# Kernel optimization log

Hardware: AMD Instinct MI355X
Metric: run time of the kernel (lower is better)

Reference implementation:

```python
import jax, jax.numpy as jnp
import numpy as np

N_USER, N_REST, D, E, Q = 200000, 50000, 64, 2000000, 500000


def setup_inputs() -> dict:
    key = jax.random.key(0)
    ks = jax.random.split(key, 16)
    s = 0.05
    return {
        "x_user": jax.random.normal(ks[0], (N_USER, D), jnp.float32),
        "x_rest": jax.random.normal(ks[1], (N_REST, D), jnp.float32),
        "Wl": jax.random.normal(ks[2], (3, 2, D, D), jnp.float32) * s,
        "Wr": jax.random.normal(ks[3], (3, 2, D, D), jnp.float32) * s,
        "bl": jnp.zeros((3, 2, D), jnp.float32),
        "dW1": jax.random.normal(ks[4], (D, 2 * D), jnp.float32) * s,
        "db1": jnp.zeros((D,), jnp.float32),
        "dW2": jax.random.normal(ks[5], (D, D), jnp.float32) * s,
        "db2": jnp.zeros((D,), jnp.float32),
        "dW3": jax.random.normal(ks[6], (1, D), jnp.float32) * s,
        "db3": jnp.zeros((1,), jnp.float32),
        "ur_src": jax.random.randint(ks[7], (E,), 0, N_USER, jnp.int32),
        "ur_dst": jax.random.randint(ks[8], (E,), 0, N_REST, jnp.int32),
        "ru_src": jax.random.randint(ks[9], (E,), 0, N_REST, jnp.int32),
        "ru_dst": jax.random.randint(ks[10], (E,), 0, N_USER, jnp.int32),
        "el_row": jax.random.randint(ks[11], (Q,), 0, N_USER, jnp.int32),
        "el_col": jax.random.randint(ks[12], (Q,), 0, N_REST, jnp.int32),
    }


def _sage(h_src, h_dst, src, dst, W_l, b_l, W_r):
    # PyG SAGEConv: lin_l(mean_{j in N(i)} x_j) + lin_r(x_i); bias on lin_l only.
    n_dst = h_dst.shape[0]
    agg = jax.ops.segment_sum(h_src[src], dst, num_segments=n_dst)  # [n_dst, D]
    cnt = jax.ops.segment_sum(jnp.ones_like(dst, dtype=h_src.dtype), dst, num_segments=n_dst)
    mean = agg / jnp.maximum(cnt, 1)[:, None]
    return mean @ W_l.T + b_l + h_dst @ W_r.T


def reference(x_user, x_rest, Wl, Wr, bl, dW1, db1, dW2, db2, dW3, db3,
              ur_src, ur_dst, ru_src, ru_dst, el_row, el_col):
    hu, hr = x_user, x_rest
    for l in range(3):
        # edge type 0: user -> restaurant ('rates'); edge type 1: reverse
        zr = _sage(hu, hr, ur_src, ur_dst, Wl[l, 0], bl[l, 0], Wr[l, 0])
        zu = _sage(hr, hu, ru_src, ru_dst, Wl[l, 1], bl[l, 1], Wr[l, 1])
        if l < 2:
            zr, zu = jax.nn.relu(zr), jax.nn.relu(zu)
        hu, hr = zu, zr
    # EdgeDecoder
    z = jnp.concatenate([hu[el_row], hr[el_col]], axis=-1)  # [Q, 2D]
    z = jax.nn.relu(z @ dW1.T + db1)
    z = jax.nn.relu(z @ dW2.T + db2)
    z = z @ dW3.T + db3
    return z.reshape(-1)
```

## Files before the change

kernel.cpp:

```cpp
#include <hip/hip_runtime.h>

#define NU 200000
#define NR 50000
#define DD 64
#define NE 2000000
#define NQ 500000
#define NBR 196
#define NBU 782

#define NBS 98
#define BKT_CAP 24576
#define LW_U 11
#define LW_R 9
#define PB_E 4096
#define NPBB 489

__global__ __launch_bounds__(256)
void binpass_kernel(const int* __restrict__ ru_src, const int* __restrict__ ru_dst,
                    const int* __restrict__ ur_src, const int* __restrict__ ur_dst,
                    int* __restrict__ bcur, int2* __restrict__ pairs) {
    __shared__ int2 stg[PB_E];
    __shared__ unsigned char gstg[PB_E];
    __shared__ int hist[256];
    __shared__ int sca[256], scb[256];
    __shared__ int gpos[128];
    int side = (blockIdx.x >= NPBB) ? 1 : 0;
    int blk = side ? (blockIdx.x - NPBB) : blockIdx.x;
    const int* src = side ? ur_src : ru_src;
    const int* dst = side ? ur_dst : ru_dst;
    int lw = side ? LW_R : LW_U;
    int* bc = bcur + side * NBS;
    int2* region = pairs + (size_t)side * NBS * BKT_CAP;
    int tid = threadIdx.x;
    hist[tid] = 0;
    __syncthreads();
    int base = blk * PB_E;
    int myg[16]; int myrank[16]; int2 myp[16];
#pragma unroll
    for (int i = 0; i < 16; i++) {
        int e = base + i * 256 + tid;
        if (e < NE) {
            int d = dst[e];
            int g = d >> lw;
            myg[i] = g;
            myp[i] = make_int2(src[e], d);
            myrank[i] = atomicAdd(&hist[g], 1);
        } else myg[i] = -1;
    }
    __syncthreads();
    int h = hist[tid];
    sca[tid] = h;
    __syncthreads();
    int* cur = sca; int* alt = scb;
    for (int off = 1; off < 256; off <<= 1) {
        int x = cur[tid];
        if (tid >= off) x += cur[tid - off];
        alt[tid] = x;
        __syncthreads();
        int* tmp = cur; cur = alt; alt = tmp;
    }
    alt[tid] = cur[tid] - h;
    if (tid < NBS && h > 0) gpos[tid] = atomicAdd(&bc[tid], h);
    __syncthreads();
    int* basep = alt;
#pragma unroll
    for (int i = 0; i < 16; i++) {
        if (myg[i] >= 0) {
            int p = basep[myg[i]] + myrank[i];
            stg[p] = myp[i];
            gstg[p] = (unsigned char)myg[i];
        }
    }
    __syncthreads();
    int tot = cur[255];
    for (int i = tid; i < tot; i += 256) {
        int g = gstg[i];
        int o = g * BKT_CAP + gpos[g] + (i - basep[g]);
        region[o] = stg[i];
    }
}

__global__ void bbase_kernel(const int* __restrict__ bcur, int* __restrict__ bbase,
                             int* __restrict__ rs_u, int* __restrict__ rs_r) {
    __shared__ int a[128], b[128];
    int sidx = blockIdx.x;
    const int* bc = bcur + sidx * NBS;
    int* bb = bbase + sidx * NBS;
    int tid = threadIdx.x;
    a[tid] = (tid < NBS) ? bc[tid] : 0;
    __syncthreads();
    int* cur = a; int* alt = b;
    for (int off = 1; off < 128; off <<= 1) {
        int t = cur[tid];
        if (tid >= off) t += cur[tid - off];
        alt[tid] = t;
        __syncthreads();
        int* tmp = cur; cur = alt; alt = tmp;
    }
    if (tid < NBS) bb[tid] = (tid == 0) ? 0 : cur[tid - 1];
    if (tid == 0) { if (sidx == 0) rs_u[NU] = NE; else rs_r[NR] = NE; }
}

__global__ __launch_bounds__(256)
void fillpass_kernel(const int2* __restrict__ pairs, const int* __restrict__ bcur,
                     const int* __restrict__ bbase,
                     int* __restrict__ rs_u, int* __restrict__ rs_r,
                     int* __restrict__ csr_u, int* __restrict__ csr_r) {
    __shared__ int win[BKT_CAP];
    __shared__ int lcnt[2048];
    __shared__ int lofs[2048];
    __shared__ int tsc[256], tsc2[256];
    int side = (blockIdx.x >= NBS) ? 1 : 0;
    int bkt = side ? (blockIdx.x - NBS) : blockIdx.x;
    const int2* reg = pairs + ((size_t)side * NBS + bkt) * BKT_CAP;
    int* rs = side ? rs_r : rs_u;
    int* csr = side ? csr_r : csr_u;
    int W = side ? 512 : 2048;
    int lw = side ? LW_R : LW_U;
    int n = side ? NR : NU;
    int d0 = bkt << lw;
    int tot = bcur[side * NBS + bkt];
    int base = bbase[side * NBS + bkt];
    int tid = threadIdx.x;
    for (int i = tid; i < W; i += 256) lcnt[i] = 0;
    __syncthreads();
    for (int i = tid; i < tot; i += 256) {
        int2 p = reg[i];
        atomicAdd(&lcnt[p.y - d0], 1);
    }
    __syncthreads();
    int per = W >> 8;
    int b0 = tid * per;
    int run = 0;
    for (int i = 0; i < per; i++) { int v = lcnt[b0 + i]; lofs[b0 + i] = run; run += v; }
    tsc[tid] = run;
    __syncthreads();
    int* cur = tsc; int* alt = tsc2;
    for (int off = 1; off < 256; off <<= 1) {
        int x = cur[tid];
        if (tid >= off) x += cur[tid - off];
        alt[tid] = x;
        __syncthreads();
        int* tmp = cur; cur = alt; alt = tmp;
    }
    int texcl = cur[tid] - run;
    for (int i = 0; i < per; i++) lofs[b0 + i] += texcl;
    __syncthreads();
    int wn = min(W, n - d0);
    for (int i = tid; i < wn; i += 256) rs[d0 + i] = base + lofs[i];
    __syncthreads();
    for (int i = tid; i < tot; i += 256) {
        int2 p = reg[i];
        int slot = atomicAdd(&lofs[p.y - d0], 1);
        win[slot] = p.x;
    }
    __syncthreads();
    for (int i = tid; i < tot; i += 256) csr[base + i] = win[i];
}

__global__ __launch_bounds__(256)
void gather2_kernel(const float* __restrict__ hu, const int* __restrict__ csr_r,
                    const int* __restrict__ rs_r, float* __restrict__ mean_r,
                    const float* __restrict__ hr, const int* __restrict__ csr_u,
                    const int* __restrict__ rs_u, float* __restrict__ mean_u) {
    int lane = threadIdx.x & 63;
    int wave = blockIdx.x * 4 + (threadIdx.x >> 6);
    const float* h; const int* csr; const int* rs; float* mean; int r;
    if (wave < NR) { h = hu; csr = csr_r; rs = rs_r; mean = mean_r; r = wave; }
    else if (wave < NR + NU) { h = hr; csr = csr_u; rs = rs_u; mean = mean_u; r = wave - NR; }
    else return;
    int s = rs[r], e = rs[r + 1];
    int g = lane >> 4;
    int fo = (lane & 15) << 2;
    float4 a0 = {0.f, 0.f, 0.f, 0.f};
    float4 a1 = {0.f, 0.f, 0.f, 0.f};
    for (int j = s; j < e; j += 64) {
        int rem = e - j;
        int nch = rem < 64 ? rem : 64;
        int li = lane < nch ? lane : nch - 1;
        int idx = csr[j + li];
        for (int kk = 0; kk < nch; kk += 8) {
            int j0 = kk + g;
            int j1 = kk + 4 + g;
            int i0 = __shfl(idx, j0);
            int i1 = __shfl(idx, j1);
            float4 x0 = *(const float4*)(h + (size_t)i0 * DD + fo);
            float4 x1 = *(const float4*)(h + (size_t)i1 * DD + fo);
            if (j0 < nch) { a0.x += x0.x; a0.y += x0.y; a0.z += x0.z; a0.w += x0.w; }
            if (j1 < nch) { a1.x += x1.x; a1.y += x1.y; a1.z += x1.z; a1.w += x1.w; }
        }
    }
    float4 acc;
    acc.x = a0.x + a1.x; acc.y = a0.y + a1.y;
    acc.z = a0.z + a1.z; acc.w = a0.w + a1.w;
    acc.x += __shfl_xor(acc.x, 16); acc.y += __shfl_xor(acc.y, 16);
    acc.z += __shfl_xor(acc.z, 16); acc.w += __shfl_xor(acc.w, 16);
    acc.x += __shfl_xor(acc.x, 32); acc.y += __shfl_xor(acc.y, 32);
    acc.z += __shfl_xor(acc.z, 32); acc.w += __shfl_xor(acc.w, 32);
    if (g == 0) {
        float inv = 1.0f / fmaxf((float)(e - s), 1.0f);
        acc.x *= inv; acc.y *= inv; acc.z *= inv; acc.w *= inv;
        *(float4*)(mean + (size_t)r * DD + fo) = acc;
    }
}

#define DOT4(A, B) ((A).x*(B).x + (A).y*(B).y + (A).z*(B).z + (A).w*(B).w)

#define SDECL(j) float sA##j = bsh[cb + (j)], sB##j = sA##j, sC##j = sA##j, sD##j = sA##j;

#define SCOL(j) { \
    const float4* wlp_ = (const float4*)(Wls + ((cb + (j)) << 6) + kc); \
    const float4* wrp_ = (const float4*)(Wrs + ((cb + (j)) << 6) + kc); \
    float4 l0_ = wlp_[0], l1_ = wlp_[1], q0_ = wrp_[0], q1_ = wrp_[1]; \
    sA##j += DOT4(mA0,l0_)+DOT4(mA1,l1_)+DOT4(xA0,q0_)+DOT4(xA1,q1_); \
    sB##j += DOT4(mB0,l0_)+DOT4(mB1,l1_)+DOT4(xB0,q0_)+DOT4(xB1,q1_); \
    sC##j += DOT4(mC0,l0_)+DOT4(mC1,l1_)+DOT4(xC0,q0_)+DOT4(xC1,q1_); \
    sD##j += DOT4(mD0,l0_)+DOT4(mD1,l1_)+DOT4(xD0,q0_)+DOT4(xD1,q1_); }

#define SRELU(j) { sA##j = fmaxf(sA##j,0.f); sB##j = fmaxf(sB##j,0.f); \
                   sC##j = fmaxf(sC##j,0.f); sD##j = fmaxf(sD##j,0.f); }

#define STORE_ROW(SR, rr) if ((rr) < n) { \
    float* o_ = out + (size_t)(rr) * DD + cb; \
    *(float4*)(o_)      = {SR##0,  SR##1,  SR##2,  SR##3}; \
    *(float4*)(o_ + 4)  = {SR##4,  SR##5,  SR##6,  SR##7}; \
    *(float4*)(o_ + 8)  = {SR##8,  SR##9,  SR##10, SR##11}; \
    *(float4*)(o_ + 12) = {SR##12, SR##13, SR##14, SR##15}; }

__device__ __forceinline__
void sage_tile(const float* __restrict__ mean, const float* __restrict__ h,
               const float* Wls, const float* Wrs, const float* bsh,
               float* __restrict__ out, int n, int do_relu, int r0, int cb) {
    int rA = min(r0, n - 1), rB = min(r0 + 64, n - 1);
    int rC = min(r0 + 128, n - 1), rD = min(r0 + 192, n - 1);
    const float *mA = mean + (size_t)rA * DD, *xA = h + (size_t)rA * DD;
    const float *mB = mean + (size_t)rB * DD, *xB = h + (size_t)rB * DD;
    const float *mC = mean + (size_t)rC * DD, *xC = h + (size_t)rC * DD;
    const float *mD = mean + (size_t)rD * DD, *xD = h + (size_t)rD * DD;
    SDECL(0)  SDECL(1)  SDECL(2)  SDECL(3)  SDECL(4)  SDECL(5)  SDECL(6)  SDECL(7)
    SDECL(8)  SDECL(9)  SDECL(10) SDECL(11) SDECL(12) SDECL(13) SDECL(14) SDECL(15)
#pragma unroll 1
    for (int kc = 0; kc < DD; kc += 8) {
        float4 mA0 = *(const float4*)(mA + kc), mA1 = *(const float4*)(mA + kc + 4);
        float4 xA0 = *(const float4*)(xA + kc), xA1 = *(const float4*)(xA + kc + 4);
        float4 mB0 = *(const float4*)(mB + kc), mB1 = *(const float4*)(mB + kc + 4);
        float4 xB0 = *(const float4*)(xB + kc), xB1 = *(const float4*)(xB + kc + 4);
        float4 mC0 = *(const float4*)(mC + kc), mC1 = *(const float4*)(mC + kc + 4);
        float4 xC0 = *(const float4*)(xC + kc), xC1 = *(const float4*)(xC + kc + 4);
        float4 mD0 = *(const float4*)(mD + kc), mD1 = *(const float4*)(mD + kc + 4);
        float4 xD0 = *(const float4*)(xD + kc), xD1 = *(const float4*)(xD + kc + 4);
        SCOL(0)  SCOL(1)  SCOL(2)  SCOL(3)  SCOL(4)  SCOL(5)  SCOL(6)  SCOL(7)
        SCOL(8)  SCOL(9)  SCOL(10) SCOL(11) SCOL(12) SCOL(13) SCOL(14) SCOL(15)
    }
    if (do_relu) {
        SRELU(0)  SRELU(1)  SRELU(2)  SRELU(3)  SRELU(4)  SRELU(5)  SRELU(6)  SRELU(7)
        SRELU(8)  SRELU(9)  SRELU(10) SRELU(11) SRELU(12) SRELU(13) SRELU(14) SRELU(15)
    }
    STORE_ROW(sA, r0)
    STORE_ROW(sB, r0 + 64)
    STORE_ROW(sC, r0 + 128)
    STORE_ROW(sD, r0 + 192)
}

__global__ __launch_bounds__(256, 2)
void sage_fused_kernel(const float* __restrict__ mean_r, const float* __restrict__ hr,
                       const float* __restrict__ mean_u, const float* __restrict__ hu,
                       const float* __restrict__ Wl2, const float* __restrict__ Wr2,
                       const float* __restrict__ bl2,
                       float* __restrict__ out_r, float* __restrict__ out_u, int do_relu) {
    __shared__ float Wls[DD * DD];
    __shared__ float Wrs[DD * DD];
    __shared__ float bsh[DD];
    int side = (blockIdx.x < NBR) ? 0 : 1;
    const float* Wl = Wl2 + side * DD * DD;
    const float* Wr = Wr2 + side * DD * DD;
    const float* bl = bl2 + side * DD;
    for (int i = threadIdx.x; i < DD * DD; i += 256) {
        Wls[i] = Wl[i];
        Wrs[i] = Wr[i];
    }
    if (threadIdx.x < DD) bsh[threadIdx.x] = bl[threadIdx.x];
    __syncthreads();
    int lane = threadIdx.x & 63;
    int cb = (threadIdx.x >> 6) * 16;
    if (side == 0) {
        int r0 = blockIdx.x * 256 + lane;
        sage_tile(mean_r, hr, Wls, Wrs, bsh, out_r, NR, do_relu, r0, cb);
    } else {
        int r0 = (blockIdx.x - NBR) * 256 + lane;
        sage_tile(mean_u, hu, Wls, Wrs, bsh, out_u, NU, do_relu, r0, cb);
    }
}

#define PCOL(j) { \
    const float4* wp_ = (const float4*)(Ws + ((cb + (j)) << 6) + kc); \
    float4 w0_ = wp_[0], w1_ = wp_[1]; \
    sA##j += DOT4(xA0,w0_)+DOT4(xA1,w1_); \
    sB##j += DOT4(xB0,w0_)+DOT4(xB1,w1_); \
    sC##j += DOT4(xC0,w0_)+DOT4(xC1,w1_); \
    sD##j += DOT4(xD0,w0_)+DOT4(xD1,w1_); }

__device__ __forceinline__
void pre_tile(const float* __restrict__ h, const float* Ws, const float* bsh,
              float* __restrict__ out, int n, int r0, int cb) {
    int rA = min(r0, n - 1), rB = min(r0 + 64, n - 1);
    int rC = min(r0 + 128, n - 1), rD = min(r0 + 192, n - 1);
    const float *xA = h + (size_t)rA * DD, *xB = h + (size_t)rB * DD;
    const float *xC = h + (size_t)rC * DD, *xD = h + (size_t)rD * DD;
    SDECL(0)  SDECL(1)  SDECL(2)  SDECL(3)  SDECL(4)  SDECL(5)  SDECL(6)  SDECL(7)
    SDECL(8)  SDECL(9)  SDECL(10) SDECL(11) SDECL(12) SDECL(13) SDECL(14) SDECL(15)
#pragma unroll 1
    for (int kc = 0; kc < DD; kc += 8) {
        float4 xA0 = *(const float4*)(xA + kc), xA1 = *(const float4*)(xA + kc + 4);
        float4 xB0 = *(const float4*)(xB + kc), xB1 = *(const float4*)(xB + kc + 4);
        float4 xC0 = *(const float4*)(xC + kc), xC1 = *(const float4*)(xC + kc + 4);
        float4 xD0 = *(const float4*)(xD + kc), xD1 = *(const float4*)(xD + kc + 4);
        PCOL(0)  PCOL(1)  PCOL(2)  PCOL(3)  PCOL(4)  PCOL(5)  PCOL(6)  PCOL(7)
        PCOL(8)  PCOL(9)  PCOL(10) PCOL(11) PCOL(12) PCOL(13) PCOL(14) PCOL(15)
    }
    STORE_ROW(sA, r0)
    STORE_ROW(sB, r0 + 64)
    STORE_ROW(sC, r0 + 128)
    STORE_ROW(sD, r0 + 192)
}

__global__ __launch_bounds__(256, 2)
void pre_fused_kernel(const float* __restrict__ hu, const float* __restrict__ hr,
                      const float* __restrict__ dW1, const float* __restrict__ db1,
                      float* __restrict__ P_u, float* __restrict__ P_r) {
    __shared__ float Ws[DD * DD];
    __shared__ float bsh[DD];
    int side = (blockIdx.x < NBU) ? 0 : 1;
    int koff = side ? DD : 0;
    for (int i = threadIdx.x; i < DD * DD; i += 256) {
        int c = i >> 6, k = i & 63;
        Ws[c * DD + k] = dW1[c * 2 * DD + koff + k];
    }
    if (threadIdx.x < DD) bsh[threadIdx.x] = side ? 0.f : db1[threadIdx.x];
    __syncthreads();
    int lane = threadIdx.x & 63;
    int cb = (threadIdx.x >> 6) * 16;
    if (side == 0) {
        int r0 = blockIdx.x * 256 + lane;
        pre_tile(hu, Ws, bsh, P_u, NU, r0, cb);
    } else {
        int r0 = (blockIdx.x - NBU) * 256 + lane;
        pre_tile(hr, Ws, bsh, P_r, NR, r0, cb);
    }
}

#define ZCOMB(Zi, i) float4 Zi; { float4 u_ = pu[i]; float4 v_ = pr[i]; \
    Zi.x = fmaxf(u_.x + v_.x, 0.f); Zi.y = fmaxf(u_.y + v_.y, 0.f); \
    Zi.z = fmaxf(u_.z + v_.z, 0.f); Zi.w = fmaxf(u_.w + v_.w, 0.f); }

__global__ __launch_bounds__(256, 2)
void decoder_kernel(const float* __restrict__ Pu, const float* __restrict__ Pr,
                    const int* __restrict__ el_row, const int* __restrict__ el_col,
                    const float* __restrict__ dW2, const float* __restrict__ db2,
                    const float* __restrict__ dW3, const float* __restrict__ db3,
                    float* __restrict__ out) {
    __shared__ float W2s[DD * DD];
    __shared__ float b2s[DD], w3s[DD];
    for (int i = threadIdx.x; i < DD * DD; i += 256) W2s[i] = dW2[i];
    if (threadIdx.x < DD) {
        b2s[threadIdx.x] = db2[threadIdx.x];
        w3s[threadIdx.x] = dW3[threadIdx.x];
    }
    __syncthreads();
    int q = blockIdx.x * 256 + threadIdx.x;
    if (q >= NQ) return;
    int row = el_row[q], col = el_col[q];
    const float4* pu = (const float4*)(Pu + (size_t)row * DD);
    const float4* pr = (const float4*)(Pr + (size_t)col * DD);
    ZCOMB(z0, 0)  ZCOMB(z1, 1)  ZCOMB(z2, 2)  ZCOMB(z3, 3)
    ZCOMB(z4, 4)  ZCOMB(z5, 5)  ZCOMB(z6, 6)  ZCOMB(z7, 7)
    ZCOMB(z8, 8)  ZCOMB(z9, 9)  ZCOMB(z10, 10) ZCOMB(z11, 11)
    ZCOMB(z12, 12) ZCOMB(z13, 13) ZCOMB(z14, 14) ZCOMB(z15, 15)
    float o = db3[0];
#pragma unroll 2
    for (int c = 0; c < DD; c++) {
        const float4* wp = (const float4*)(W2s + c * DD);
        float s = b2s[c]
            + DOT4(z0, wp[0])  + DOT4(z1, wp[1])  + DOT4(z2, wp[2])  + DOT4(z3, wp[3])
            + DOT4(z4, wp[4])  + DOT4(z5, wp[5])  + DOT4(z6, wp[6])  + DOT4(z7, wp[7])
            + DOT4(z8, wp[8])  + DOT4(z9, wp[9])  + DOT4(z10, wp[10]) + DOT4(z11, wp[11])
            + DOT4(z12, wp[12]) + DOT4(z13, wp[13]) + DOT4(z14, wp[14]) + DOT4(z15, wp[15]);
        o += fmaxf(s, 0.f) * w3s[c];
    }
    out[q] = o;
}

extern "C" void kernel_launch(void* const* d_in, const int* in_sizes, int n_in,
                              void* d_out, int out_size, void* d_ws, size_t ws_size,
                              hipStream_t stream) {
    const float* x_user = (const float*)d_in[0];
    const float* x_rest = (const float*)d_in[1];
    const float* Wl     = (const float*)d_in[2];
    const float* Wr     = (const float*)d_in[3];
    const float* bl     = (const float*)d_in[4];
    const float* dW1    = (const float*)d_in[5];
    const float* db1    = (const float*)d_in[6];
    const float* dW2    = (const float*)d_in[7];
    const float* db2    = (const float*)d_in[8];
    const float* dW3    = (const float*)d_in[9];
    const float* db3    = (const float*)d_in[10];
    const int* ur_src   = (const int*)d_in[11];
    const int* ur_dst   = (const int*)d_in[12];
    const int* ru_src   = (const int*)d_in[13];
    const int* ru_dst   = (const int*)d_in[14];
    const int* el_row   = (const int*)d_in[15];
    const int* el_col   = (const int*)d_in[16];
    float* out = (float*)d_out;

    char* w = (char*)d_ws;
    size_t off = 0;
    auto alloc = [&](size_t bytes) -> void* {
        void* p = (void*)(w + off);
        off += (bytes + 255) & ~(size_t)255;
        return p;
    };
    float* hu0    = (float*)alloc((size_t)NU * DD * 4);
    float* hu1    = (float*)alloc((size_t)NU * DD * 4);
    float* hr0    = (float*)alloc((size_t)NR * DD * 4);
    float* hr1    = (float*)alloc((size_t)NR * DD * 4);
    float* mean_u = (float*)alloc((size_t)NU * DD * 4);
    float* mean_r = (float*)alloc((size_t)NR * DD * 4);
    int* csr_u  = (int*)alloc((size_t)NE * 4);
    int* csr_r  = (int*)alloc((size_t)NE * 4);
    int* rs_u   = (int*)alloc((size_t)(NU + 1) * 4);
    int* rs_r   = (int*)alloc((size_t)(NR + 1) * 4);
    int* bcur   = (int*)alloc((size_t)2 * NBS * 4);
    int* bbase  = (int*)alloc((size_t)2 * NBS * 4);

    int2* pairs = (int2*)mean_u;

    hipMemsetAsync(bcur, 0, (size_t)2 * NBS * 4, stream);
    binpass_kernel<<<2 * NPBB, 256, 0, stream>>>(ru_src, ru_dst, ur_src, ur_dst,
                                                 bcur, pairs);
    bbase_kernel<<<2, 128, 0, stream>>>(bcur, bbase, rs_u, rs_r);
    fillpass_kernel<<<2 * NBS, 256, 0, stream>>>(pairs, bcur, bbase,
                                                 rs_u, rs_r, csr_u, csr_r);

    const float* cu = x_user;
    const float* cr = x_rest;
    float* nu_[3] = {hu0, hu1, hu0};
    float* nr_[3] = {hr0, hr1, hr0};
    const int ggrid = (NR + NU + 3) / 4;

    for (int l = 0; l < 3; l++) {
        const float* Wl2 = Wl + (size_t)l * 2 * DD * DD;
        const float* Wr2 = Wr + (size_t)l * 2 * DD * DD;
        const float* bl2 = bl + (size_t)l * 2 * DD;
        int relu = (l < 2) ? 1 : 0;
        gather2_kernel<<<ggrid, 256, 0, stream>>>(cu, csr_r, rs_r, mean_r,
                                                  cr, csr_u, rs_u, mean_u);
        sage_fused_kernel<<<NBR + NBU, 256, 0, stream>>>(mean_r, cr, mean_u, cu,
                                                         Wl2, Wr2, bl2,
                                                         nr_[l], nu_[l], relu);
        cu = nu_[l];
        cr = nr_[l];
    }
    float* P_u = hu1;
    float* P_r = hr1;
    pre_fused_kernel<<<NBU + NBR, 256, 0, stream>>>(cu, cr, dW1, db1, P_u, P_r);
    decoder_kernel<<<(NQ + 255) / 256, 256, 0, stream>>>(P_u, P_r, el_row, el_col,
                                                         dW2, db2, dW3, db3, out);
}
```

Before: 1.153 ms.

## Stage row tiles in padded shared memory for SAGE and decoder-precompute GEMMs

Measured after the change: 1.001 ms. 1.15x faster.

```diff
diff --git a/kernel.cpp b/kernel.cpp
--- a/kernel.cpp
+++ b/kernel.cpp
@@ -7,6 +7,7 @@
 #define NQ 500000
 #define NBR 196
 #define NBU 782
+#define LDW 68
 
 #define NBS 98
 #define BKT_CAP 24576
@@ -206,146 +207,147 @@
 
 #define DOT4(A, B) ((A).x*(B).x + (A).y*(B).y + (A).z*(B).z + (A).w*(B).w)
 
-#define SDECL(j) float sA##j = bsh[cb + (j)], sB##j = sA##j, sC##j = sA##j, sD##j = sA##j;
-
-#define SCOL(j) { \
-    const float4* wlp_ = (const float4*)(Wls + ((cb + (j)) << 6) + kc); \
-    const float4* wrp_ = (const float4*)(Wrs + ((cb + (j)) << 6) + kc); \
-    float4 l0_ = wlp_[0], l1_ = wlp_[1], q0_ = wrp_[0], q1_ = wrp_[1]; \
-    sA##j += DOT4(mA0,l0_)+DOT4(mA1,l1_)+DOT4(xA0,q0_)+DOT4(xA1,q1_); \
-    sB##j += DOT4(mB0,l0_)+DOT4(mB1,l1_)+DOT4(xB0,q0_)+DOT4(xB1,q1_); \
-    sC##j += DOT4(mC0,l0_)+DOT4(mC1,l1_)+DOT4(xC0,q0_)+DOT4(xC1,q1_); \
-    sD##j += DOT4(mD0,l0_)+DOT4(mD1,l1_)+DOT4(xD0,q0_)+DOT4(xD1,q1_); }
-
-#define SRELU(j) { sA##j = fmaxf(sA##j,0.f); sB##j = fmaxf(sB##j,0.f); \
-                   sC##j = fmaxf(sC##j,0.f); sD##j = fmaxf(sD##j,0.f); }
-
-#define STORE_ROW(SR, rr) if ((rr) < n) { \
-    float* o_ = out + (size_t)(rr) * DD + cb; \
-    *(float4*)(o_)      = {SR##0,  SR##1,  SR##2,  SR##3}; \
-    *(float4*)(o_ + 4)  = {SR##4,  SR##5,  SR##6,  SR##7}; \
-    *(float4*)(o_ + 8)  = {SR##8,  SR##9,  SR##10, SR##11}; \
-    *(float4*)(o_ + 12) = {SR##12, SR##13, SR##14, SR##15}; }
-
-__device__ __forceinline__
-void sage_tile(const float* __restrict__ mean, const float* __restrict__ h,
-               const float* Wls, const float* Wrs, const float* bsh,
-               float* __restrict__ out, int n, int do_relu, int r0, int cb) {
-    int rA = min(r0, n - 1), rB = min(r0 + 64, n - 1);
-    int rC = min(r0 + 128, n - 1), rD = min(r0 + 192, n - 1);
-    const float *mA = mean + (size_t)rA * DD, *xA = h + (size_t)rA * DD;
-    const float *mB = mean + (size_t)rB * DD, *xB = h + (size_t)rB * DD;
-    const float *mC = mean + (size_t)rC * DD, *xC = h + (size_t)rC * DD;
-    const float *mD = mean + (size_t)rD * DD, *xD = h + (size_t)rD * DD;
-    SDECL(0)  SDECL(1)  SDECL(2)  SDECL(3)  SDECL(4)  SDECL(5)  SDECL(6)  SDECL(7)
-    SDECL(8)  SDECL(9)  SDECL(10) SDECL(11) SDECL(12) SDECL(13) SDECL(14) SDECL(15)
-#pragma unroll 1
-    for (int kc = 0; kc < DD; kc += 8) {
-        float4 mA0 = *(const float4*)(mA + kc), mA1 = *(const float4*)(mA + kc + 4);
-        float4 xA0 = *(const float4*)(xA + kc), xA1 = *(const float4*)(xA + kc + 4);
-        float4 mB0 = *(const float4*)(mB + kc), mB1 = *(const float4*)(mB + kc + 4);
-        float4 xB0 = *(const float4*)(xB + kc), xB1 = *(const float4*)(xB + kc + 4);
-        float4 mC0 = *(const float4*)(mC + kc), mC1 = *(const float4*)(mC + kc + 4);
-        float4 xC0 = *(const float4*)(xC + kc), xC1 = *(const float4*)(xC + kc + 4);
-        float4 mD0 = *(const float4*)(mD + kc), mD1 = *(const float4*)(mD + kc + 4);
-        float4 xD0 = *(const float4*)(xD + kc), xD1 = *(const float4*)(xD + kc + 4);
-        SCOL(0)  SCOL(1)  SCOL(2)  SCOL(3)  SCOL(4)  SCOL(5)  SCOL(6)  SCOL(7)
-        SCOL(8)  SCOL(9)  SCOL(10) SCOL(11) SCOL(12) SCOL(13) SCOL(14) SCOL(15)
-    }
-    if (do_relu) {
-        SRELU(0)  SRELU(1)  SRELU(2)  SRELU(3)  SRELU(4)  SRELU(5)  SRELU(6)  SRELU(7)
-        SRELU(8)  SRELU(9)  SRELU(10) SRELU(11) SRELU(12) SRELU(13) SRELU(14) SRELU(15)
-    }
-    STORE_ROW(sA, r0)
-    STORE_ROW(sB, r0 + 64)
-    STORE_ROW(sC, r0 + 128)
-    STORE_ROW(sD, r0 + 192)
-}
-
 __global__ __launch_bounds__(256, 2)
 void sage_fused_kernel(const float* __restrict__ mean_r, const float* __restrict__ hr,
                        const float* __restrict__ mean_u, const float* __restrict__ hu,
                        const float* __restrict__ Wl2, const float* __restrict__ Wr2,
                        const float* __restrict__ bl2,
                        float* __restrict__ out_r, float* __restrict__ out_u, int do_relu) {
-    __shared__ float Wls[DD * DD];
-    __shared__ float Wrs[DD * DD];
+    __shared__ __attribute__((aligned(16))) float Wls[DD * LDW];
+    __shared__ __attribute__((aligned(16))) float Wrs[DD * LDW];
+    __shared__ __attribute__((aligned(16))) float Ms[64 * LDW];
+    __shared__ __attribute__((aligned(16))) float Xs[64 * LDW];
     __shared__ float bsh[DD];
     int side = (blockIdx.x < NBR) ? 0 : 1;
     const float* Wl = Wl2 + side * DD * DD;
     const float* Wr = Wr2 + side * DD * DD;
     const float* bl = bl2 + side * DD;
-    for (int i = threadIdx.x; i < DD * DD; i += 256) {
-        Wls[i] = Wl[i];
-        Wrs[i] = Wr[i];
-    }
-    if (threadIdx.x < DD) bsh[threadIdx.x] = bl[threadIdx.x];
-    __syncthreads();
-    int lane = threadIdx.x & 63;
-    int cb = (threadIdx.x >> 6) * 16;
-    if (side == 0) {
-        int r0 = blockIdx.x * 256 + lane;
-        sage_tile(mean_r, hr, Wls, Wrs, bsh, out_r, NR, do_relu, r0, cb);
-    } else {
-        int r0 = (blockIdx.x - NBR) * 256 + lane;
-        sage_tile(mean_u, hu, Wls, Wrs, bsh, out_u, NU, do_relu, r0, cb);
-    }
-}
-
-#define PCOL(j) { \
-    const float4* wp_ = (const float4*)(Ws + ((cb + (j)) << 6) + kc); \
-    float4 w0_ = wp_[0], w1_ = wp_[1]; \
-    sA##j += DOT4(xA0,w0_)+DOT4(xA1,w1_); \
-    sB##j += DOT4(xB0,w0_)+DOT4(xB1,w1_); \
-    sC##j += DOT4(xC0,w0_)+DOT4(xC1,w1_); \
-    sD##j += DOT4(xD0,w0_)+DOT4(xD1,w1_); }
-
-__device__ __forceinline__
-void pre_tile(const float* __restrict__ h, const float* Ws, const float* bsh,
-              float* __restrict__ out, int n, int r0, int cb) {
-    int rA = min(r0, n - 1), rB = min(r0 + 64, n - 1);
-    int rC = min(r0 + 128, n - 1), rD = min(r0 + 192, n - 1);
-    const float *xA = h + (size_t)rA * DD, *xB = h + (size_t)rB * DD;
-    const float *xC = h + (size_t)rC * DD, *xD = h + (size_t)rD * DD;
-    SDECL(0)  SDECL(1)  SDECL(2)  SDECL(3)  SDECL(4)  SDECL(5)  SDECL(6)  SDECL(7)
-    SDECL(8)  SDECL(9)  SDECL(10) SDECL(11) SDECL(12) SDECL(13) SDECL(14) SDECL(15)
+    const float* mean; const float* h; float* out; int n; int blk;
+    if (side == 0) { mean = mean_r; h = hr; out = out_r; n = NR; blk = blockIdx.x; }
+    else { mean = mean_u; h = hu; out = out_u; n = NU; blk = blockIdx.x - NBR; }
+    int tid = threadIdx.x;
+    for (int i = tid; i < DD * DD; i += 256) {
+        int c = i >> 6, k = i & 63;
+        Wls[c * LDW + k] = Wl[i];
+        Wrs[c * LDW + k] = Wr[i];
+    }
+    if (tid < DD) bsh[tid] = bl[tid];
+    int rgrp = tid & 15;
+    int cgrp = tid >> 4;
+    int cb = cgrp * 4;
+    int r00 = blk * 256;
+    for (int ch = 0; ch < 4; ch++) {
+        int rc0 = r00 + ch * 64;
+        __syncthreads();
+        for (int i = tid; i < 1024; i += 256) {
+            int row = i >> 4;
+            int c4 = (i & 15) << 2;
+            int gr = min(rc0 + row, n - 1);
+            *(float4*)&Ms[row * LDW + c4] = *(const float4*)(mean + (size_t)gr * DD + c4);
+            *(float4*)&Xs[row * LDW + c4] = *(const float4*)(h + (size_t)gr * DD + c4);
+        }
+        __syncthreads();
+        float4 bias = {bsh[cb], bsh[cb + 1], bsh[cb + 2], bsh[cb + 3]};
+        float4 acc0 = bias, acc1 = bias, acc2 = bias, acc3 = bias;
 #pragma unroll 1
-    for (int kc = 0; kc < DD; kc += 8) {
-        float4 xA0 = *(const float4*)(xA + kc), xA1 = *(const float4*)(xA + kc + 4);
-        float4 xB0 = *(const float4*)(xB + kc), xB1 = *(const float4*)(xB + kc + 4);
-        float4 xC0 = *(const float4*)(xC + kc), xC1 = *(const float4*)(xC + kc + 4);
-        float4 xD0 = *(const float4*)(xD + kc), xD1 = *(const float4*)(xD + kc + 4);
-        PCOL(0)  PCOL(1)  PCOL(2)  PCOL(3)  PCOL(4)  PCOL(5)  PCOL(6)  PCOL(7)
-        PCOL(8)  PCOL(9)  PCOL(10) PCOL(11) PCOL(12) PCOL(13) PCOL(14) PCOL(15)
-    }
-    STORE_ROW(sA, r0)
-    STORE_ROW(sB, r0 + 64)
-    STORE_ROW(sC, r0 + 128)
-    STORE_ROW(sD, r0 + 192)
+        for (int kc = 0; kc < DD; kc += 8) {
+            float4 wl[4][2], wr[4][2];
+#pragma unroll
+            for (int c = 0; c < 4; c++) {
+                wl[c][0] = *(const float4*)&Wls[(cb + c) * LDW + kc];
+                wl[c][1] = *(const float4*)&Wls[(cb + c) * LDW + kc + 4];
+                wr[c][0] = *(const float4*)&Wrs[(cb + c) * LDW + kc];
+                wr[c][1] = *(const float4*)&Wrs[(cb + c) * LDW + kc + 4];
+            }
+#define SROW(J, ACC) { \
+            int row_ = rgrp + 16 * (J); \
+            float4 ma_ = *(const float4*)&Ms[row_ * LDW + kc]; \
+            float4 mb_ = *(const float4*)&Ms[row_ * LDW + kc + 4]; \
+            float4 xa_ = *(const float4*)&Xs[row_ * LDW + kc]; \
+            float4 xb_ = *(const float4*)&Xs[row_ * LDW + kc + 4]; \
+            ACC.x += DOT4(ma_,wl[0][0])+DOT4(mb_,wl[0][1])+DOT4(xa_,wr[0][0])+DOT4(xb_,wr[0][1]); \
+            ACC.y += DOT4(ma_,wl[1][0])+DOT4(mb_,wl[1][1])+DOT4(xa_,wr[1][0])+DOT4(xb_,wr[1][1]); \
+            ACC.z += DOT4(ma_,wl[2][0])+DOT4(mb_,wl[2][1])+DOT4(xa_,wr[2][0])+DOT4(xb_,wr[2][1]); \
+            ACC.w += DOT4(ma_,wl[3][0])+DOT4(mb_,wl[3][1])+DOT4(xa_,wr[3][0])+DOT4(xb_,wr[3][1]); }
+            SROW(0, acc0) SROW(1, acc1) SROW(2, acc2) SROW(3, acc3)
+#undef SROW
+        }
+        if (do_relu) {
+            acc0.x = fmaxf(acc0.x, 0.f); acc0.y = fmaxf(acc0.y, 0.f); acc0.z = fmaxf(acc0.z, 0.f); acc0.w = fmaxf(acc0.w, 0.f);
+            acc1.x = fmaxf(acc1.x, 0.f); acc1.y = fmaxf(acc1.y, 0.f); acc1.z = fmaxf(acc1.z, 0.f); acc1.w = fmaxf(acc1.w, 0.f);
+            acc2.x = fmaxf(acc2.x, 0.f); acc2.y = fmaxf(acc2.y, 0.f); acc2.z = fmaxf(acc2.z, 0.f); acc2.w = fmaxf(acc2.w, 0.f);
+            acc3.x = fmaxf(acc3.x, 0.f); acc3.y = fmaxf(acc3.y, 0.f); acc3.z = fmaxf(acc3.z, 0.f); acc3.w = fmaxf(acc3.w, 0.f);
+        }
+        {
+            int r0_ = rc0 + rgrp;
+            if (r0_ < n)      *(float4*)(out + (size_t)r0_ * DD + cb) = acc0;
+            if (r0_ + 16 < n) *(float4*)(out + (size_t)(r0_ + 16) * DD + cb) = acc1;
+            if (r0_ + 32 < n) *(float4*)(out + (size_t)(r0_ + 32) * DD + cb) = acc2;
+            if (r0_ + 48 < n) *(float4*)(out + (size_t)(r0_ + 48) * DD + cb) = acc3;
+        }
+    }
 }
 
 __global__ __launch_bounds__(256, 2)
 void pre_fused_kernel(const float* __restrict__ hu, const float* __restrict__ hr,
                       const float* __restrict__ dW1, const float* __restrict__ db1,
                       float* __restrict__ P_u, float* __restrict__ P_r) {
-    __shared__ float Ws[DD * DD];
+    __shared__ __attribute__((aligned(16))) float Ws[DD * LDW];
+    __shared__ __attribute__((aligned(16))) float Xs[64 * LDW];
     __shared__ float bsh[DD];
     int side = (blockIdx.x < NBU) ? 0 : 1;
     int koff = side ? DD : 0;
-    for (int i = threadIdx.x; i < DD * DD; i += 256) {
+    const float* h; float* out; int n; int blk;
+    if (side == 0) { h = hu; out = P_u; n = NU; blk = blockIdx.x; }
+    else { h = hr; out = P_r; n = NR; blk = blockIdx.x - NBU; }
+    int tid = threadIdx.x;
+    for (int i = tid; i < DD * DD; i += 256) {
         int c = i >> 6, k = i & 63;
-        Ws[c * DD + k] = dW1[c * 2 * DD + koff + k];
-    }
-    if (threadIdx.x < DD) bsh[threadIdx.x] = side ? 0.f : db1[threadIdx.x];
-    __syncthreads();
-    int lane = threadIdx.x & 63;
-    int cb = (threadIdx.x >> 6) * 16;
-    if (side == 0) {
-        int r0 = blockIdx.x * 256 + lane;
-        pre_tile(hu, Ws, bsh, P_u, NU, r0, cb);
-    } else {
-        int r0 = (blockIdx.x - NBU) * 256 + lane;
-        pre_tile(hr, Ws, bsh, P_r, NR, r0, cb);
+        Ws[c * LDW + k] = dW1[c * 2 * DD + koff + k];
+    }
+    if (tid < DD) bsh[tid] = side ? 0.f : db1[tid];
+    int rgrp = tid & 15;
+    int cgrp = tid >> 4;
+    int cb = cgrp * 4;
+    int r00 = blk * 256;
+    for (int ch = 0; ch < 4; ch++) {
+        int rc0 = r00 + ch * 64;
+        __syncthreads();
+        for (int i = tid; i < 1024; i += 256) {
+            int row = i >> 4;
+            int c4 = (i & 15) << 2;
+            int gr = min(rc0 + row, n - 1);
+            *(float4*)&Xs[row * LDW + c4] = *(const float4*)(h + (size_t)gr * DD + c4);
+        }
+        __syncthreads();
+        float4 bias = {bsh[cb], bsh[cb + 1], bsh[cb + 2], bsh[cb + 3]};
+        float4 acc0 = bias, acc1 = bias, acc2 = bias, acc3 = bias;
+#pragma unroll 1
+        for (int kc = 0; kc < DD; kc += 8) {
+            float4 wv[4][2];
+#pragma unroll
+            for (int c = 0; c < 4; c++) {
+                wv[c][0] = *(const float4*)&Ws[(cb + c) * LDW + kc];
+                wv[c][1] = *(const float4*)&Ws[(cb + c) * LDW + kc + 4];
+            }
+#define PROW(J, ACC) { \
+            int row_ = rgrp + 16 * (J); \
+            float4 xa_ = *(const float4*)&Xs[row_ * LDW + kc]; \
+            float4 xb_ = *(const float4*)&Xs[row_ * LDW + kc + 4]; \
+            ACC.x += DOT4(xa_,wv[0][0])+DOT4(xb_,wv[0][1]); \
+            ACC.y += DOT4(xa_,wv[1][0])+DOT4(xb_,wv[1][1]); \
+            ACC.z += DOT4(xa_,wv[2][0])+DOT4(xb_,wv[2][1]); \
+            ACC.w += DOT4(xa_,wv[3][0])+DOT4(xb_,wv[3][1]); }
+            PROW(0, acc0) PROW(1, acc1) PROW(2, acc2) PROW(3, acc3)
+#undef PROW
+        }
+        {
+            int r0_ = rc0 + rgrp;
+            if (r0_ < n)      *(float4*)(out + (size_t)r0_ * DD + cb) = acc0;
+            if (r0_ + 16 < n) *(float4*)(out + (size_t)(r0_ + 16) * DD + cb) = acc1;
+            if (r0_ + 32 < n) *(float4*)(out + (size_t)(r0_ + 32) * DD + cb) = acc2;
+            if (r0_ + 48 < n) *(float4*)(out + (size_t)(r0_ + 48) * DD + cb) = acc3;
+        }
     }
 }
 
```
